# Performance work log

Measured on AMD Instinct MI355X. Metric: run time of the kernel, lower is better.

## Reference

```python
import jax, jax.numpy as jnp
import numpy as np

B, IN, OUT = 8192, 4096, 4096


def setup_inputs() -> dict:
    key = jax.random.key(0)
    k_x, k_w, k_t, k_n = jax.random.split(key, 4)
    # int8 activations and weights (stored as int8; accumulated in int32)
    x = jax.random.randint(k_x, (B, IN), -128, 128, dtype=jnp.int32).astype(jnp.int8)
    W = jax.random.randint(k_w, (OUT, IN), -128, 128, dtype=jnp.int32).astype(jnp.int8)
    # per-channel BN fold: additive term t (int32) and negative bitshift n
    t = jax.random.randint(k_t, (OUT,), -(1 << 15), 1 << 15, dtype=jnp.int32)
    n = jax.random.randint(k_n, (OUT,), -9, -6, dtype=jnp.int32)  # shift right by 6..8
    act_min = jnp.full((OUT,), -128, dtype=jnp.int32)
    act_max = jnp.full((OUT,), 127, dtype=jnp.int32)
    return {"x": x, "W": W, "t": t, "n": n, "act_min": act_min, "act_max": act_max}


def reference(x, W, t, n, act_min, act_max):
    # int32-accumulate int8 GEMM: F.linear(x, W) -> [B, OUT]
    acc = jnp.matmul(x.astype(jnp.int32), W.astype(jnp.int32).T)
    acc = acc + t  # broadcast per-output-channel bias add
    acc = jnp.right_shift(acc, -n)  # arithmetic right shift requantization
    acc = jnp.clip(acc, act_min, act_max)
    # pure_positive is False (act_min < 0) -> cast to small signed type
    return acc.astype(jnp.int8)
```

## Files before the change

### kernel.cpp

```cpp
#include <hip/hip_runtime.h>
#include <stdint.h>


#define BDIM 8192
#define INDIM 4096
#define OUTDIM 4096

typedef __attribute__((ext_vector_type(4))) int I4;

__global__ __launch_bounds__(256) void pack_i32_to_i8(const int* __restrict__ src,
                                                      uint32_t* __restrict__ dst, int n4) {
    int idx = blockIdx.x * 256 + threadIdx.x;
    if (idx >= n4) return;
    int4 a = ((const int4*)src)[idx];
    uint32_t p = ((uint32_t)a.x & 255u)
               | (((uint32_t)a.y & 255u) << 8)
               | (((uint32_t)a.z & 255u) << 16)
               | (((uint32_t)a.w & 255u) << 24);
    dst[idx] = p;
}

__global__ __launch_bounds__(256) void gemm_i8_fused(
    const uint8_t* __restrict__ Xp,
    const uint8_t* __restrict__ Wp,
    const int* __restrict__ t, const int* __restrict__ nsh,
    const int* __restrict__ amin, const int* __restrict__ amax,
    int* __restrict__ out) {

    __shared__ uint8_t sA[128 * 64];
    __shared__ uint8_t sB[128 * 64];

    const int bn = blockIdx.x;
    const int bm = blockIdx.y;
    const int tid = threadIdx.x;
    const int w = tid >> 6;
    const int lane = tid & 63;
    const int wm = (w & 1) * 64;
    const int wn = (w >> 1) * 64;

    const int lrow = lane >> 2;
    const int lcol = (lane & 3) * 16;

    const uint8_t* gA0 = Xp + (size_t)(bm * 128) * INDIM;
    const uint8_t* gB0 = Wp + (size_t)(bn * 128) * INDIM;

    I4 acc[4][4];
#pragma unroll
    for (int i = 0; i < 4; ++i)
#pragma unroll
        for (int j = 0; j < 4; ++j) acc[i][j] = (I4){0, 0, 0, 0};

    const int quad = lane >> 4;
    const int rl = lane & 15;

    for (int k0 = 0; k0 < INDIM; k0 += 64) {
#pragma unroll
        for (int r = 0; r < 2; ++r) {
            const int c = r * 4 + w;
            const int row = c * 16 + lrow;
            __builtin_amdgcn_global_load_lds(
                (const __attribute__((address_space(1))) uint32_t*)(gA0 + (size_t)row * INDIM + k0 + lcol),
                (__attribute__((address_space(3))) uint32_t*)(sA + c * 1024 + lane * 16),
                16, 0, 0);
            __builtin_amdgcn_global_load_lds(
                (const __attribute__((address_space(1))) uint32_t*)(gB0 + (size_t)row * INDIM + k0 + lcol),
                (__attribute__((address_space(3))) uint32_t*)(sB + c * 1024 + lane * 16),
                16, 0, 0);
        }
        __syncthreads();

        I4 af[4], bf[4];
#pragma unroll
        for (int i = 0; i < 4; ++i)
            af[i] = *(const I4*)(sA + (wm + i * 16 + rl) * 64 + quad * 16);
#pragma unroll
        for (int j = 0; j < 4; ++j)
            bf[j] = *(const I4*)(sB + (wn + j * 16 + rl) * 64 + quad * 16);

#pragma unroll
        for (int i = 0; i < 4; ++i)
#pragma unroll
            for (int j = 0; j < 4; ++j)
                acc[i][j] = __builtin_amdgcn_mfma_i32_16x16x64_i8(af[i], bf[j], acc[i][j], 0, 0, 0);

        __syncthreads();
    }

#pragma unroll
    for (int j = 0; j < 4; ++j) {
        const int o = bn * 128 + wn + j * 16 + rl;
        const int tt = t[o];
        const int sh = -nsh[o];
        const int mn = amin[o];
        const int mx = amax[o];
#pragma unroll
        for (int i = 0; i < 4; ++i) {
            const int rowbase = bm * 128 + wm + i * 16 + quad * 4;
#pragma unroll
            for (int r = 0; r < 4; ++r) {
                int v = acc[i][j][r] + tt;
                v >>= sh;
                v = v < mn ? mn : (v > mx ? mx : v);
                out[(size_t)(rowbase + r) * OUTDIM + o] = v;
            }
        }
    }
}

extern "C" void kernel_launch(void* const* d_in, const int* in_sizes, int n_in,
                              void* d_out, int out_size, void* d_ws, size_t ws_size,
                              hipStream_t stream) {
    const int* x = (const int*)d_in[0];
    const int* W = (const int*)d_in[1];
    const int* t = (const int*)d_in[2];
    const int* n = (const int*)d_in[3];
    const int* amin = (const int*)d_in[4];
    const int* amax = (const int*)d_in[5];
    int* out = (int*)d_out;

    uint8_t* xp = (uint8_t*)d_ws;
    uint8_t* wp = xp + (size_t)BDIM * INDIM;

    {
        int n4 = BDIM * INDIM / 4;
        pack_i32_to_i8<<<n4 / 256, 256, 0, stream>>>(x, (uint32_t*)xp, n4);
    }
    {
        int n4 = OUTDIM * INDIM / 4;
        pack_i32_to_i8<<<n4 / 256, 256, 0, stream>>>(W, (uint32_t*)wp, n4);
    }

    dim3 grid(OUTDIM / 128, BDIM / 128);
    gemm_i8_fused<<<grid, 256, 0, stream>>>(xp, wp, t, n, amin, amax, out);
}
```

Before: 422.6 us.

## Double K-tile depth with XOR-swizzled LDS, merge pack kernels, nontemporal stores

The GEMM K step grows from 64 to 128, which halves the number of barrier pairs per tile, and the LDS layout now uses an XOR swizzle on 16-byte chunks to avoid bank conflicts on fragment reads. The two int32-to-int8 pack kernels become one launch in which each thread packs 16 elements with a 16-byte store. Output stores are made nontemporal. LDS use doubles to 32KB per block, which may reduce occupancy.

```diff
diff --git a/kernel.cpp b/kernel.cpp
--- a/kernel.cpp
+++ b/kernel.cpp
@@ -8,16 +8,32 @@
 
 typedef __attribute__((ext_vector_type(4))) int I4;
 
-__global__ __launch_bounds__(256) void pack_i32_to_i8(const int* __restrict__ src,
-                                                      uint32_t* __restrict__ dst, int n4) {
-    int idx = blockIdx.x * 256 + threadIdx.x;
-    if (idx >= n4) return;
-    int4 a = ((const int4*)src)[idx];
-    uint32_t p = ((uint32_t)a.x & 255u)
-               | (((uint32_t)a.y & 255u) << 8)
-               | (((uint32_t)a.z & 255u) << 16)
-               | (((uint32_t)a.w & 255u) << 24);
-    dst[idx] = p;
+__global__ __launch_bounds__(256) void pack_both(const int* __restrict__ x,
+                                                 const int* __restrict__ W,
+                                                 uint32_t* __restrict__ xp,
+                                                 uint32_t* __restrict__ wp) {
+    const size_t xq = (size_t)BDIM * INDIM / 16;
+    size_t idx = (size_t)blockIdx.x * 256 + threadIdx.x;
+    const int* src;
+    uint32_t* dst;
+    if (idx < xq) {
+        src = x + idx * 16;
+        dst = xp + idx * 4;
+    } else {
+        size_t j = idx - xq;
+        src = W + j * 16;
+        dst = wp + j * 4;
+    }
+    uint32_t outw[4];
+#pragma unroll
+    for (int q = 0; q < 4; ++q) {
+        int4 a = ((const int4*)src)[q];
+        outw[q] = ((uint32_t)a.x & 255u)
+                | (((uint32_t)a.y & 255u) << 8)
+                | (((uint32_t)a.z & 255u) << 16)
+                | (((uint32_t)a.w & 255u) << 24);
+    }
+    *(uint4*)dst = *(uint4*)outw;
 }
 
 __global__ __launch_bounds__(256) void gemm_i8_fused(
@@ -27,8 +43,8 @@
     const int* __restrict__ amin, const int* __restrict__ amax,
     int* __restrict__ out) {
 
-    __shared__ uint8_t sA[128 * 64];
-    __shared__ uint8_t sB[128 * 64];
+    __shared__ uint8_t sA[128 * 128];
+    __shared__ uint8_t sB[128 * 128];
 
     const int bn = blockIdx.x;
     const int bm = blockIdx.y;
@@ -38,8 +54,9 @@
     const int wm = (w & 1) * 64;
     const int wn = (w >> 1) * 64;
 
-    const int lrow = lane >> 2;
-    const int lcol = (lane & 3) * 16;
+    const int lrow8 = lane >> 3;
+    const int gk16 = (lane & 7) ^ lrow8;
+    const int gcol = gk16 * 16;
 
     const uint8_t* gA0 = Xp + (size_t)(bm * 128) * INDIM;
     const uint8_t* gB0 = Wp + (size_t)(bn * 128) * INDIM;
@@ -52,37 +69,41 @@
 
     const int quad = lane >> 4;
     const int rl = lane & 15;
+    const int swz = rl & 7;
 
-    for (int k0 = 0; k0 < INDIM; k0 += 64) {
+    for (int k0 = 0; k0 < INDIM; k0 += 128) {
 #pragma unroll
-        for (int r = 0; r < 2; ++r) {
+        for (int r = 0; r < 4; ++r) {
             const int c = r * 4 + w;
-            const int row = c * 16 + lrow;
+            const int row = c * 8 + lrow8;
             __builtin_amdgcn_global_load_lds(
-                (const __attribute__((address_space(1))) uint32_t*)(gA0 + (size_t)row * INDIM + k0 + lcol),
+                (const __attribute__((address_space(1))) uint32_t*)(gA0 + (size_t)row * INDIM + k0 + gcol),
                 (__attribute__((address_space(3))) uint32_t*)(sA + c * 1024 + lane * 16),
                 16, 0, 0);
             __builtin_amdgcn_global_load_lds(
-                (const __attribute__((address_space(1))) uint32_t*)(gB0 + (size_t)row * INDIM + k0 + lcol),
+                (const __attribute__((address_space(1))) uint32_t*)(gB0 + (size_t)row * INDIM + k0 + gcol),
                 (__attribute__((address_space(3))) uint32_t*)(sB + c * 1024 + lane * 16),
                 16, 0, 0);
         }
         __syncthreads();
 
-        I4 af[4], bf[4];
 #pragma unroll
-        for (int i = 0; i < 4; ++i)
-            af[i] = *(const I4*)(sA + (wm + i * 16 + rl) * 64 + quad * 16);
+        for (int s = 0; s < 2; ++s) {
+            const int koff = ((s * 4 + quad) ^ swz) * 16;
+            I4 af[4], bf[4];
 #pragma unroll
-        for (int j = 0; j < 4; ++j)
-            bf[j] = *(const I4*)(sB + (wn + j * 16 + rl) * 64 + quad * 16);
+            for (int i = 0; i < 4; ++i)
+                af[i] = *(const I4*)(sA + (wm + i * 16 + rl) * 128 + koff);
+#pragma unroll
+            for (int j = 0; j < 4; ++j)
+                bf[j] = *(const I4*)(sB + (wn + j * 16 + rl) * 128 + koff);
 
 #pragma unroll
-        for (int i = 0; i < 4; ++i)
+            for (int i = 0; i < 4; ++i)
 #pragma unroll
-            for (int j = 0; j < 4; ++j)
-                acc[i][j] = __builtin_amdgcn_mfma_i32_16x16x64_i8(af[i], bf[j], acc[i][j], 0, 0, 0);
-
+                for (int j = 0; j < 4; ++j)
+                    acc[i][j] = __builtin_amdgcn_mfma_i32_16x16x64_i8(af[i], bf[j], acc[i][j], 0, 0, 0);
+        }
         __syncthreads();
     }
 
@@ -101,7 +122,7 @@
                 int v = acc[i][j][r] + tt;
                 v >>= sh;
                 v = v < mn ? mn : (v > mx ? mx : v);
-                out[(size_t)(rowbase + r) * OUTDIM + o] = v;
+                __builtin_nontemporal_store(v, &out[(size_t)(rowbase + r) * OUTDIM + o]);
             }
         }
     }
@@ -122,12 +143,8 @@
     uint8_t* wp = xp + (size_t)BDIM * INDIM;
 
     {
-        int n4 = BDIM * INDIM / 4;
-        pack_i32_to_i8<<<n4 / 256, 256, 0, stream>>>(x, (uint32_t*)xp, n4);
-    }
-    {
-        int n4 = OUTDIM * INDIM / 4;
-        pack_i32_to_i8<<<n4 / 256, 256, 0, stream>>>(W, (uint32_t*)wp, n4);
+        int nthreads = (BDIM * (INDIM / 16)) + (OUTDIM * (INDIM / 16));
+        pack_both<<<nthreads / 256, 256, 0, stream>>>(x, W, (uint32_t*)xp, (uint32_t*)wp);
     }
 
     dim3 grid(OUTDIM / 128, BDIM / 128);
```

Measured after the change: 428.8 us. Within noise of the previous version (+1.5%).

## Enlarge GEMM tile to 256x256, overlap next-k loads, merge pack kernels

Applied to the files above, without the earlier changes.

Grows the block tile from 128x128 to 256x256 with 512 threads, and each wave now computes 128x64 outputs, which raises operand reuse and cuts global traffic per MFMA. The next k-slice is issued into the single LDS buffer after a barrier, so the global loads overlap with the MFMA work on fragments already held in registers. The two int32-to-int8 pack kernels are merged into one launch, and the output stores become nontemporal. In exchange the accumulator count doubles, which adds register pressure and may lower occupancy, and the grid shrinks to 512 blocks.

```diff
diff --git a/kernel.cpp b/kernel.cpp
--- a/kernel.cpp
+++ b/kernel.cpp
@@ -8,77 +8,96 @@
 
 typedef __attribute__((ext_vector_type(4))) int I4;
 
-__global__ __launch_bounds__(256) void pack_i32_to_i8(const int* __restrict__ src,
-                                                      uint32_t* __restrict__ dst, int n4) {
-    int idx = blockIdx.x * 256 + threadIdx.x;
-    if (idx >= n4) return;
-    int4 a = ((const int4*)src)[idx];
-    uint32_t p = ((uint32_t)a.x & 255u)
-               | (((uint32_t)a.y & 255u) << 8)
-               | (((uint32_t)a.z & 255u) << 16)
-               | (((uint32_t)a.w & 255u) << 24);
-    dst[idx] = p;
+__global__ __launch_bounds__(256) void pack_both(const int* __restrict__ x,
+                                                 const int* __restrict__ W,
+                                                 uint32_t* __restrict__ dst) {
+    const uint32_t xq = (uint32_t)BDIM * (INDIM / 4);
+    uint32_t base = blockIdx.x * 1024;
+    const int4* src4 = (base < xq) ? ((const int4*)x + base)
+                                   : ((const int4*)W + (base - xq));
+#pragma unroll
+    for (int q = 0; q < 4; ++q) {
+        uint32_t off = threadIdx.x + q * 256;
+        int4 a = src4[off];
+        dst[base + off] = ((uint32_t)a.x & 255u)
+                        | (((uint32_t)a.y & 255u) << 8)
+                        | (((uint32_t)a.z & 255u) << 16)
+                        | (((uint32_t)a.w & 255u) << 24);
+    }
 }
 
-__global__ __launch_bounds__(256) void gemm_i8_fused(
+__global__ __launch_bounds__(512, 2) void gemm_i8_fused(
     const uint8_t* __restrict__ Xp,
     const uint8_t* __restrict__ Wp,
     const int* __restrict__ t, const int* __restrict__ nsh,
     const int* __restrict__ amin, const int* __restrict__ amax,
     int* __restrict__ out) {
 
-    __shared__ uint8_t sA[128 * 64];
-    __shared__ uint8_t sB[128 * 64];
+    __shared__ uint8_t sA[256 * 64];
+    __shared__ uint8_t sB[256 * 64];
 
     const int bn = blockIdx.x;
     const int bm = blockIdx.y;
     const int tid = threadIdx.x;
     const int w = tid >> 6;
     const int lane = tid & 63;
-    const int wm = (w & 1) * 64;
-    const int wn = (w >> 1) * 64;
+    const int wrow = (w >> 2) * 128;
+    const int wcol = (w & 3) * 64;
+    const int quad = lane >> 4;
+    const int rl = lane & 15;
 
     const int lrow = lane >> 2;
     const int lcol = (lane & 3) * 16;
 
-    const uint8_t* gA0 = Xp + (size_t)(bm * 128) * INDIM;
-    const uint8_t* gB0 = Wp + (size_t)(bn * 128) * INDIM;
+    const uint8_t* gA = Xp + (size_t)(bm * 256) * INDIM;
+    const uint8_t* gB = Wp + (size_t)(bn * 256) * INDIM;
+    const int c0 = 2 * w, c1 = 2 * w + 1;
+    const uint8_t* gA0 = gA + (size_t)(c0 * 16 + lrow) * INDIM + lcol;
+    const uint8_t* gA1 = gA + (size_t)(c1 * 16 + lrow) * INDIM + lcol;
+    const uint8_t* gB0 = gB + (size_t)(c0 * 16 + lrow) * INDIM + lcol;
+    const uint8_t* gB1 = gB + (size_t)(c1 * 16 + lrow) * INDIM + lcol;
+    __attribute__((address_space(3))) uint32_t* dA0 =
+        (__attribute__((address_space(3))) uint32_t*)(sA + c0 * 1024 + lane * 16);
+    __attribute__((address_space(3))) uint32_t* dA1 =
+        (__attribute__((address_space(3))) uint32_t*)(sA + c1 * 1024 + lane * 16);
+    __attribute__((address_space(3))) uint32_t* dB0 =
+        (__attribute__((address_space(3))) uint32_t*)(sB + c0 * 1024 + lane * 16);
+    __attribute__((address_space(3))) uint32_t* dB1 =
+        (__attribute__((address_space(3))) uint32_t*)(sB + c1 * 1024 + lane * 16);
 
-    I4 acc[4][4];
+    __builtin_amdgcn_global_load_lds((const __attribute__((address_space(1))) uint32_t*)gA0, dA0, 16, 0, 0);
+    __builtin_amdgcn_global_load_lds((const __attribute__((address_space(1))) uint32_t*)gA1, dA1, 16, 0, 0);
+    __builtin_amdgcn_global_load_lds((const __attribute__((address_space(1))) uint32_t*)gB0, dB0, 16, 0, 0);
+    __builtin_amdgcn_global_load_lds((const __attribute__((address_space(1))) uint32_t*)gB1, dB1, 16, 0, 0);
+    __syncthreads();
+
+    I4 acc[8][4];
 #pragma unroll
-    for (int i = 0; i < 4; ++i)
+    for (int i = 0; i < 8; ++i)
 #pragma unroll
         for (int j = 0; j < 4; ++j) acc[i][j] = (I4){0, 0, 0, 0};
 
-    const int quad = lane >> 4;
-    const int rl = lane & 15;
+    for (int it = 0; it < 64; ++it) {
+        I4 af[8], bf[4];
+#pragma unroll
+        for (int i = 0; i < 8; ++i)
+            af[i] = *(const I4*)(sA + (wrow + i * 16 + rl) * 64 + quad * 16);
+#pragma unroll
+        for (int j = 0; j < 4; ++j)
+            bf[j] = *(const I4*)(sB + (wcol + j * 16 + rl) * 64 + quad * 16);
 
-    for (int k0 = 0; k0 < INDIM; k0 += 64) {
-#pragma unroll
-        for (int r = 0; r < 2; ++r) {
-            const int c = r * 4 + w;
-            const int row = c * 16 + lrow;
-            __builtin_amdgcn_global_load_lds(
-                (const __attribute__((address_space(1))) uint32_t*)(gA0 + (size_t)row * INDIM + k0 + lcol),
-                (__attribute__((address_space(3))) uint32_t*)(sA + c * 1024 + lane * 16),
-                16, 0, 0);
-            __builtin_amdgcn_global_load_lds(
-                (const __attribute__((address_space(1))) uint32_t*)(gB0 + (size_t)row * INDIM + k0 + lcol),
-                (__attribute__((address_space(3))) uint32_t*)(sB + c * 1024 + lane * 16),
-                16, 0, 0);
-        }
         __syncthreads();
 
-        I4 af[4], bf[4];
-#pragma unroll
-        for (int i = 0; i < 4; ++i)
-            af[i] = *(const I4*)(sA + (wm + i * 16 + rl) * 64 + quad * 16);
-#pragma unroll
-        for (int j = 0; j < 4; ++j)
-            bf[j] = *(const I4*)(sB + (wn + j * 16 + rl) * 64 + quad * 16);
+        if (it < 63) {
+            const size_t ko = (size_t)(it + 1) * 64;
+            __builtin_amdgcn_global_load_lds((const __attribute__((address_space(1))) uint32_t*)(gA0 + ko), dA0, 16, 0, 0);
+            __builtin_amdgcn_global_load_lds((const __attribute__((address_space(1))) uint32_t*)(gA1 + ko), dA1, 16, 0, 0);
+            __builtin_amdgcn_global_load_lds((const __attribute__((address_space(1))) uint32_t*)(gB0 + ko), dB0, 16, 0, 0);
+            __builtin_amdgcn_global_load_lds((const __attribute__((address_space(1))) uint32_t*)(gB1 + ko), dB1, 16, 0, 0);
+        }
 
 #pragma unroll
-        for (int i = 0; i < 4; ++i)
+        for (int i = 0; i < 8; ++i)
 #pragma unroll
             for (int j = 0; j < 4; ++j)
                 acc[i][j] = __builtin_amdgcn_mfma_i32_16x16x64_i8(af[i], bf[j], acc[i][j], 0, 0, 0);
@@ -88,20 +107,20 @@
 
 #pragma unroll
     for (int j = 0; j < 4; ++j) {
-        const int o = bn * 128 + wn + j * 16 + rl;
+        const int o = bn * 256 + wcol + j * 16 + rl;
         const int tt = t[o];
         const int sh = -nsh[o];
         const int mn = amin[o];
         const int mx = amax[o];
 #pragma unroll
-        for (int i = 0; i < 4; ++i) {
-            const int rowbase = bm * 128 + wm + i * 16 + quad * 4;
+        for (int i = 0; i < 8; ++i) {
+            const int rowbase = bm * 256 + wrow + i * 16 + quad * 4;
 #pragma unroll
             for (int r = 0; r < 4; ++r) {
                 int v = acc[i][j][r] + tt;
                 v >>= sh;
                 v = v < mn ? mn : (v > mx ? mx : v);
-                out[(size_t)(rowbase + r) * OUTDIM + o] = v;
+                __builtin_nontemporal_store(v, &out[(size_t)(rowbase + r) * OUTDIM + o]);
             }
         }
     }
@@ -122,14 +141,10 @@
     uint8_t* wp = xp + (size_t)BDIM * INDIM;
 
     {
-        int n4 = BDIM * INDIM / 4;
-        pack_i32_to_i8<<<n4 / 256, 256, 0, stream>>>(x, (uint32_t*)xp, n4);
-    }
-    {
-        int n4 = OUTDIM * INDIM / 4;
-        pack_i32_to_i8<<<n4 / 256, 256, 0, stream>>>(W, (uint32_t*)wp, n4);
+        int nblocks = ((BDIM + OUTDIM) * (INDIM / 4)) / 1024;
+        pack_both<<<nblocks, 256, 0, stream>>>(x, W, (uint32_t*)d_ws);
     }
 
-    dim3 grid(OUTDIM / 128, BDIM / 128);
-    gemm_i8_fused<<<grid, 256, 0, stream>>>(xp, wp, t, n, amin, amax, out);
+    dim3 grid(OUTDIM / 256, BDIM / 256);
+    gemm_i8_fused<<<grid, 512, 0, stream>>>(xp, wp, t, n, amin, amax, out);
 }
```

Measured after the change: 430.9 us. About the same (+2.0%).
